# Optimization experiments

Hardware: AMD Instinct MI355X
Metric: run time of the kernel (lower is better)

## Reference

```python
import jax, jax.numpy as jnp
import numpy as np

D_MODEL = 1024
N_HEADS = 16
HEAD_DIM = D_MODEL // N_HEADS
SCALE = HEAD_DIM ** -0.5
MASK_FILL = -10000.0


def setup_inputs() -> dict:
    key = jax.random.key(0)
    ks = jax.random.split(key, 12)
    B, L, D = 2, 2048, D_MODEL
    inv = 1.0 / np.sqrt(D)
    inp = {
        "query": jax.random.normal(ks[0], (B, L, D), jnp.float32),
        "key": jax.random.normal(ks[1], (B, L, D), jnp.float32),
        "value": jax.random.normal(ks[2], (B, L, D), jnp.float32),
        "Wq": jax.random.normal(ks[3], (D, D), jnp.float32) * inv,
        "bq": jnp.zeros((D,), jnp.float32),
        "Wk": jax.random.normal(ks[4], (D, D), jnp.float32) * inv,
        "bk": jnp.zeros((D,), jnp.float32),
        "Wv": jax.random.normal(ks[5], (D, D), jnp.float32) * inv,
        "bv": jnp.zeros((D,), jnp.float32),
        "Wo": jax.random.normal(ks[6], (D, D), jnp.float32) * inv,
        "bo": jnp.zeros((D,), jnp.float32),
        "valid_mask": jax.random.randint(ks[7], (B, L), 0, 2).astype(jnp.bool_),
    }
    return inp


def reference(query, key, value, Wq, bq, Wk, bk, Wv, bv, Wo, bo, valid_mask):
    B, Lq, D = query.shape
    Lk = key.shape[1]
    H, HD = N_HEADS, HEAD_DIM
    # torch.nn.Linear: y = x @ W.T + b
    Q = (query @ Wq.T + bq).reshape(B, Lq, H, HD).transpose(0, 2, 1, 3)  # [B,H,Lq,HD]
    K = (key @ Wk.T + bk).reshape(B, Lk, H, HD).transpose(0, 2, 1, 3)    # [B,H,Lk,HD]
    V = (value @ Wv.T + bv).reshape(B, Lk, H, HD).transpose(0, 2, 1, 3)  # [B,H,Lk,HD]
    scores = jnp.einsum("bhqd,bhkd->bhqk", Q, K) * SCALE
    scores = jnp.where(valid_mask[:, None, None, :], scores, MASK_FILL)
    weights = jax.nn.softmax(scores, axis=-1)  # dropout is identity at inference
    out = jnp.einsum("bhqk,bhkd->bhqd", weights, V)
    out = out.transpose(0, 2, 1, 3).reshape(B, Lq, D)
    out = out @ Wo.T + bo
    # zero rows of fully-invalid batches
    gate = jnp.any(valid_mask, axis=1).astype(out.dtype)[:, None, None]
    return out * gate
```

## Files before the change

### kernel.cpp

```cpp
#include <hip/hip_runtime.h>
#include <hip/hip_bf16.h>

typedef __hip_bfloat16 bf16;
typedef __attribute__((ext_vector_type(8))) short s8v;
typedef __attribute__((ext_vector_type(4))) float f4v;

#define LOG2E 1.44269504088896340736f
#define CSCALE (0.125f * LOG2E)
#define MASK_B2 (-14426.950408889634f)
#define NEG_BIG (-30000.0f)

#define BB 2
#define LL 2048
#define DD 1024
#define HH 16
#define HD 64
#define MTOT 4096
#define PER_T 4194304

struct alignas(8) B4 { bf16 v[4]; };

__device__ __forceinline__ void async_cp16(const bf16* g, bf16* l) {
    __builtin_amdgcn_global_load_lds(
        (const __attribute__((address_space(1))) void*)g,
        (__attribute__((address_space(3))) void*)l, 16, 0, 0);
}

struct CvtArgs {
    const float* src[7];
    bf16* dst[7];
    int n[7];
};

__global__ __launch_bounds__(256) void cvt_kernel(CvtArgs args) {
    const int which = blockIdx.y;
    const float* __restrict__ src = args.src[which];
    bf16* __restrict__ dst = args.dst[which];
    const int n4 = args.n[which] >> 2;
    const int stride = gridDim.x * 256;
    for (int i = blockIdx.x * 256 + threadIdx.x; i < n4; i += stride) {
        const float4 f = ((const float4*)src)[i];
        B4 o;
        o.v[0] = __float2bfloat16(f.x);
        o.v[1] = __float2bfloat16(f.y);
        o.v[2] = __float2bfloat16(f.z);
        o.v[3] = __float2bfloat16(f.w);
        ((B4*)dst)[i] = o;
    }
}

struct QkvArgs {
    const bf16* A[3];
    const bf16* W[3];
    const float* bias[3];
    bf16* out[3];
};

template <int FUSED>
__global__ __launch_bounds__(256) void gemm128(QkvArgs qa,
                                               const bf16* __restrict__ Ao,
                                               const bf16* __restrict__ Wo_,
                                               const float* __restrict__ bo_,
                                               float* __restrict__ out_f,
                                               const int* __restrict__ mask) {
    __shared__ bf16 sA[128 * 64];
    __shared__ bf16 sB[128 * 64];
    __shared__ int sgate;

    const int which = FUSED ? blockIdx.z : 0;
    const bf16* __restrict__ A = FUSED ? qa.A[which] : Ao;
    const bf16* __restrict__ W = FUSED ? qa.W[which] : Wo_;
    const float* __restrict__ bias = FUSED ? qa.bias[which] : bo_;
    bf16* __restrict__ out_bf = FUSED ? qa.out[which] : nullptr;

    const int lane = threadIdx.x & 63;
    const int w = threadIdx.x >> 6;
    const int lr = lane & 15;
    const int quad = lane >> 4;
    const int wr = w >> 1, wc = w & 1;
    const int rbase = blockIdx.x * 128;
    const int cbase = blockIdx.y * 128;
    const int dma_r = lane >> 3;
    const int dma_cc = ((lane & 7) ^ dma_r) * 8;

    if (!FUSED) {
        if (threadIdx.x == 0) sgate = 0;
        __syncthreads();
        const int b_ = rbase >> 11;
        int any = 0;
        for (int i = threadIdx.x; i < LL; i += 256) any |= mask[b_ * LL + i];
        if (any) sgate = 1;
    }

    f4v acc[4][4] = {};
    for (int kt = 0; kt < DD / 64; kt++) {
        const int k0 = kt * 64;
        __syncthreads();
#pragma unroll
        for (int t = 0; t < 4; t++) {
            const int g = w * 4 + t;
            async_cp16(A + (size_t)(rbase + g * 8 + dma_r) * DD + k0 + dma_cc,
                       &sA[g * 512]);
            async_cp16(W + (size_t)(cbase + g * 8 + dma_r) * DD + k0 + dma_cc,
                       &sB[g * 512]);
        }
        __syncthreads();
#pragma unroll
        for (int s = 0; s < 2; s++) {
            s8v a[4], b[4];
#pragma unroll
            for (int i = 0; i < 4; i++) {
                const int row = wr * 64 + i * 16 + lr;
                a[i] = *(const s8v*)&sA[row * 64 + (((s * 4 + quad) ^ (row & 7)) * 8)];
            }
#pragma unroll
            for (int j = 0; j < 4; j++) {
                const int row = wc * 64 + j * 16 + lr;
                b[j] = *(const s8v*)&sB[row * 64 + (((s * 4 + quad) ^ (row & 7)) * 8)];
            }
#pragma unroll
            for (int i = 0; i < 4; i++)
#pragma unroll
                for (int j = 0; j < 4; j++)
                    acc[i][j] = __builtin_amdgcn_mfma_f32_16x16x32_bf16(a[i], b[j], acc[i][j], 0, 0, 0);
        }
    }

    const float gatef = (!FUSED) ? (sgate ? 1.0f : 0.0f) : 1.0f;

#pragma unroll
    for (int j = 0; j < 4; j++) {
        const int n = cbase + wc * 64 + j * 16 + lr;
        const float bv = bias[n];
#pragma unroll
        for (int i = 0; i < 4; i++) {
#pragma unroll
            for (int r = 0; r < 4; r++) {
                const int m = rbase + wr * 64 + i * 16 + quad * 4 + r;
                const float v = acc[i][j][r] + bv;
                if (!FUSED) {
                    out_f[(size_t)m * DD + n] = v * gatef;
                } else {
                    const int b_ = m >> 11, l = m & (LL - 1);
                    const int h = n >> 6, hd = n & 63;
                    if (which == 2)
                        out_bf[(((size_t)(b_ * HH + h)) * HD + hd) * LL + l] = __float2bfloat16(v);
                    else
                        out_bf[(((size_t)(b_ * HH + h)) * LL + l) * HD + hd] = __float2bfloat16(v);
                }
            }
        }
    }
}

__global__ __launch_bounds__(512) void attn_kernel(const bf16* __restrict__ Q,
                                                   const bf16* __restrict__ K,
                                                   const bf16* __restrict__ Vt,
                                                   const int* __restrict__ mask,
                                                   bf16* __restrict__ Aout) {
    __shared__ bf16 sK[2][64 * 64];
    __shared__ bf16 sV[2][64 * 64];
    __shared__ bf16 sP[8][16 * 72];
    __shared__ float sBias[LL];

    const int lane = threadIdx.x & 63;
    const int w = threadIdx.x >> 6;
    const int lr = lane & 15;
    const int quad = lane >> 4;

    const int bid = blockIdx.x;
    const int qb = bid & 15;
    const int h = (bid >> 4) & 15;
    const int b = bid >> 8;

    const size_t head_off = ((size_t)(b * HH + h)) * LL * HD;
    const bf16* Qh = Q + head_off;
    const bf16* Kh = K + head_off;
    const bf16* Vh = Vt + head_off;
    const int q0 = qb * 128 + w * 16;

    const int dma_r = lane >> 3;
    const int dma_cc = ((lane & 7) ^ dma_r) * 8;
    const int sw = lr & 7;

    {
        const int* mb = mask + b * LL;
        for (int i = threadIdx.x; i < LL; i += 512)
            sBias[i] = mb[i] ? 0.0f : MASK_B2;
        async_cp16(Kh + (size_t)(w * 8 + dma_r) * HD + dma_cc, &sK[0][w * 512]);
        async_cp16(Vh + (size_t)(w * 8 + dma_r) * LL + dma_cc, &sV[0][w * 512]);
    }
    __syncthreads();

    const s8v aq0 = *(const s8v*)(Qh + (size_t)(q0 + lr) * HD + quad * 8);
    const s8v aq1 = *(const s8v*)(Qh + (size_t)(q0 + lr) * HD + 32 + quad * 8);

    bf16* sPw = &sP[w][0];
    f4v O[4] = {};
    float mrun = NEG_BIG, lrun = 0.0f;

    int asrc[4];
#pragma unroll
    for (int r = 0; r < 4; r++) asrc[r] = (lane & 48) | (quad * 4 + r);

    for (int kt = 0; kt < LL / 64; kt++) {
        const int kbase = kt * 64;
        const bf16* kb = &sK[kt & 1][0];
        const bf16* vb = &sV[kt & 1][0];

        if (kt < LL / 64 - 1) {
            const int nb = (kt + 1) & 1;
            async_cp16(Kh + (size_t)(kbase + 64 + w * 8 + dma_r) * HD + dma_cc,
                       &sK[nb][w * 512]);
            async_cp16(Vh + (size_t)(w * 8 + dma_r) * LL + kbase + 64 + dma_cc,
                       &sV[nb][w * 512]);
        }

        f4v T[4];
#pragma unroll
        for (int j = 0; j < 4; j++) {
            const int row = 16 * j + lr;
            const s8v kb0 = *(const s8v*)&kb[row * 64 + ((quad ^ sw) * 8)];
            const s8v kb1 = *(const s8v*)&kb[row * 64 + (((quad + 4) ^ sw) * 8)];
            f4v t = {};
            t = __builtin_amdgcn_mfma_f32_16x16x32_bf16(kb0, aq0, t, 0, 0, 0);
            T[j] = __builtin_amdgcn_mfma_f32_16x16x32_bf16(kb1, aq1, t, 0, 0, 0);
        }

        s8v v0[4], v1[4];
#pragma unroll
        for (int dt = 0; dt < 4; dt++) {
            const int vrow = dt * 16 + lr;
            v0[dt] = *(const s8v*)&vb[vrow * 64 + ((quad ^ sw) * 8)];
            v1[dt] = *(const s8v*)&vb[vrow * 64 + (((quad + 4) ^ sw) * 8)];
        }

        float mloc = NEG_BIG;
#pragma unroll
        for (int j = 0; j < 4; j++) {
            const f4v bj = *(const f4v*)&sBias[kbase + j * 16 + quad * 4];
#pragma unroll
            for (int r = 0; r < 4; r++) {
                T[j][r] = T[j][r] * CSCALE + bj[r];
                mloc = fmaxf(mloc, T[j][r]);
            }
        }
        mloc = fmaxf(mloc, __shfl_xor(mloc, 16));
        mloc = fmaxf(mloc, __shfl_xor(mloc, 32));

        if (__any(mloc > mrun)) {
            const float mnew = fmaxf(mrun, mloc);
            const float alphaq = exp2f(mrun - mnew);
            mrun = mnew;
            lrun *= alphaq;
            float aB[4];
#pragma unroll
            for (int r = 0; r < 4; r++) aB[r] = __shfl(alphaq, asrc[r]);
#pragma unroll
            for (int dt = 0; dt < 4; dt++)
#pragma unroll
                for (int r = 0; r < 4; r++) O[dt][r] *= aB[r];
        }

        float ls = 0.0f;
#pragma unroll
        for (int j = 0; j < 4; j++)
#pragma unroll
            for (int r = 0; r < 4; r++) {
                const float e = exp2f(T[j][r] - mrun);
                T[j][r] = e;
                ls += e;
            }
        ls += __shfl_xor(ls, 16);
        ls += __shfl_xor(ls, 32);
        lrun += ls;

        asm volatile("" ::: "memory");
#pragma unroll
        for (int j = 0; j < 4; j++) {
            B4 pk;
            pk.v[0] = __float2bfloat16(T[j][0]);
            pk.v[1] = __float2bfloat16(T[j][1]);
            pk.v[2] = __float2bfloat16(T[j][2]);
            pk.v[3] = __float2bfloat16(T[j][3]);
            *(B4*)&sPw[lr * 72 + j * 16 + quad * 4] = pk;
        }
        asm volatile("s_waitcnt lgkmcnt(0)" ::: "memory");
        const s8v pa0 = *(const s8v*)(sPw + lr * 72 + quad * 8);
        const s8v pa1 = *(const s8v*)(sPw + lr * 72 + 32 + quad * 8);

#pragma unroll
        for (int dt = 0; dt < 4; dt++) {
            O[dt] = __builtin_amdgcn_mfma_f32_16x16x32_bf16(pa0, v0[dt], O[dt], 0, 0, 0);
            O[dt] = __builtin_amdgcn_mfma_f32_16x16x32_bf16(pa1, v1[dt], O[dt], 0, 0, 0);
        }

        __syncthreads();
    }

    const float linv = 1.0f / lrun;
    float lB[4];
#pragma unroll
    for (int r = 0; r < 4; r++) lB[r] = __shfl(linv, asrc[r]);
#pragma unroll
    for (int dt = 0; dt < 4; dt++)
#pragma unroll
        for (int r = 0; r < 4; r++) {
            const int q = q0 + quad * 4 + r;
            Aout[((size_t)(b * LL + q)) * DD + h * HD + dt * 16 + lr] =
                __float2bfloat16(O[dt][r] * lB[r]);
        }
}

extern "C" void kernel_launch(void* const* d_in, const int* in_sizes, int n_in,
                              void* d_out, int out_size, void* d_ws, size_t ws_size,
                              hipStream_t stream) {
    const float* query = (const float*)d_in[0];
    const float* key   = (const float*)d_in[1];
    const float* value = (const float*)d_in[2];
    const float* Wq = (const float*)d_in[3];
    const float* bq = (const float*)d_in[4];
    const float* Wk = (const float*)d_in[5];
    const float* bk = (const float*)d_in[6];
    const float* Wv = (const float*)d_in[7];
    const float* bv = (const float*)d_in[8];
    const float* Wo = (const float*)d_in[9];
    const float* bo = (const float*)d_in[10];
    const int* mask = (const int*)d_in[11];

    bf16* base = (bf16*)d_ws;
    bf16* qx = base;
    bf16* kx = qx + PER_T;
    bf16* vx = kx + PER_T;
    bf16* wq = vx + PER_T;
    bf16* wk = wq + DD * DD;
    bf16* wv = wk + DD * DD;
    bf16* wo = wv + DD * DD;
    bf16* Qs = wo + DD * DD;
    bf16* Ks = Qs + PER_T;
    bf16* Vst = Ks + PER_T;
    bf16* aws = Vst + PER_T;

    CvtArgs ca;
    ca.src[0] = query; ca.dst[0] = qx; ca.n[0] = PER_T;
    ca.src[1] = key;   ca.dst[1] = kx; ca.n[1] = PER_T;
    ca.src[2] = value; ca.dst[2] = vx; ca.n[2] = PER_T;
    ca.src[3] = Wq;    ca.dst[3] = wq; ca.n[3] = DD * DD;
    ca.src[4] = Wk;    ca.dst[4] = wk; ca.n[4] = DD * DD;
    ca.src[5] = Wv;    ca.dst[5] = wv; ca.n[5] = DD * DD;
    ca.src[6] = Wo;    ca.dst[6] = wo; ca.n[6] = DD * DD;
    cvt_kernel<<<dim3(1024, 7), 256, 0, stream>>>(ca);

    QkvArgs qa;
    qa.A[0] = qx; qa.W[0] = wq; qa.bias[0] = bq; qa.out[0] = Qs;
    qa.A[1] = kx; qa.W[1] = wk; qa.bias[1] = bk; qa.out[1] = Ks;
    qa.A[2] = vx; qa.W[2] = wv; qa.bias[2] = bv; qa.out[2] = Vst;

    gemm128<1><<<dim3(MTOT / 128, DD / 128, 3), 256, 0, stream>>>(
        qa, nullptr, nullptr, nullptr, nullptr, nullptr);

    attn_kernel<<<BB * HH * (LL / 128), 512, 0, stream>>>(Qs, Ks, Vst, mask, aws);

    QkvArgs dummy{};
    gemm128<0><<<dim3(MTOT / 128, DD / 128, 1), 256, 0, stream>>>(
        dummy, aws, wo, bo, (float*)d_out, mask);
}
```

Before: 267.3 us.

## Vectorize GEMM epilogue stores via MFMA operand swap and LDS-staged transpose

Swaps the MFMA operands so each lane holds four consecutive output columns, which lets the Wo projection write float4 stores and the Q/K projections stage tiles through padded LDS. The V projection, whose output is transposed, is also staged through LDS. All head-layout outputs are then written back as 16-byte coalesced rows instead of scattered 2-byte stores. This costs an extra LDS round trip and a barrier in the epilogue and reuses the operand LDS buffer.

Result: faster. 258.1 us (-3.4%).

```diff
diff --git a/kernel.cpp b/kernel.cpp
--- a/kernel.cpp
+++ b/kernel.cpp
@@ -56,22 +56,16 @@
     bf16* out[3];
 };
 
-template <int FUSED>
-__global__ __launch_bounds__(256) void gemm128(QkvArgs qa,
-                                               const bf16* __restrict__ Ao,
-                                               const bf16* __restrict__ Wo_,
-                                               const float* __restrict__ bo_,
-                                               float* __restrict__ out_f,
-                                               const int* __restrict__ mask) {
-    __shared__ bf16 sA[128 * 64];
-    __shared__ bf16 sB[128 * 64];
-    __shared__ int sgate;
-
-    const int which = FUSED ? blockIdx.z : 0;
-    const bf16* __restrict__ A = FUSED ? qa.A[which] : Ao;
-    const bf16* __restrict__ W = FUSED ? qa.W[which] : Wo_;
-    const float* __restrict__ bias = FUSED ? qa.bias[which] : bo_;
-    bf16* __restrict__ out_bf = FUSED ? qa.out[which] : nullptr;
+template <int FUSED, int SWAP>
+__device__ __forceinline__ void gemm_body(const bf16* __restrict__ A,
+                                          const bf16* __restrict__ W,
+                                          const float* __restrict__ bias,
+                                          bf16* __restrict__ out_bf,
+                                          float* __restrict__ out_f,
+                                          float gatef, char* smem) {
+    bf16* sA = (bf16*)smem;
+    bf16* sB = (bf16*)(smem + 128 * 64 * 2);
+    bf16* sE = (bf16*)smem;
 
     const int lane = threadIdx.x & 63;
     const int w = threadIdx.x >> 6;
@@ -83,15 +77,6 @@
     const int dma_r = lane >> 3;
     const int dma_cc = ((lane & 7) ^ dma_r) * 8;
 
-    if (!FUSED) {
-        if (threadIdx.x == 0) sgate = 0;
-        __syncthreads();
-        const int b_ = rbase >> 11;
-        int any = 0;
-        for (int i = threadIdx.x; i < LL; i += 256) any |= mask[b_ * LL + i];
-        if (any) sgate = 1;
-    }
-
     f4v acc[4][4] = {};
     for (int kt = 0; kt < DD / 64; kt++) {
         const int k0 = kt * 64;
@@ -122,34 +107,126 @@
             for (int i = 0; i < 4; i++)
 #pragma unroll
                 for (int j = 0; j < 4; j++)
-                    acc[i][j] = __builtin_amdgcn_mfma_f32_16x16x32_bf16(a[i], b[j], acc[i][j], 0, 0, 0);
-        }
-    }
-
-    const float gatef = (!FUSED) ? (sgate ? 1.0f : 0.0f) : 1.0f;
-
-#pragma unroll
-    for (int j = 0; j < 4; j++) {
-        const int n = cbase + wc * 64 + j * 16 + lr;
-        const float bv = bias[n];
-#pragma unroll
-        for (int i = 0; i < 4; i++) {
-#pragma unroll
-            for (int r = 0; r < 4; r++) {
-                const int m = rbase + wr * 64 + i * 16 + quad * 4 + r;
-                const float v = acc[i][j][r] + bv;
-                if (!FUSED) {
-                    out_f[(size_t)m * DD + n] = v * gatef;
-                } else {
-                    const int b_ = m >> 11, l = m & (LL - 1);
-                    const int h = n >> 6, hd = n & 63;
-                    if (which == 2)
-                        out_bf[(((size_t)(b_ * HH + h)) * HD + hd) * LL + l] = __float2bfloat16(v);
-                    else
-                        out_bf[(((size_t)(b_ * HH + h)) * LL + l) * HD + hd] = __float2bfloat16(v);
-                }
-            }
-        }
+                    acc[i][j] = SWAP
+                        ? __builtin_amdgcn_mfma_f32_16x16x32_bf16(b[j], a[i], acc[i][j], 0, 0, 0)
+                        : __builtin_amdgcn_mfma_f32_16x16x32_bf16(a[i], b[j], acc[i][j], 0, 0, 0);
+        }
+    }
+    __syncthreads();
+
+    if (FUSED == 0) {
+#pragma unroll
+        for (int j = 0; j < 4; j++) {
+            const int n = cbase + wc * 64 + j * 16 + quad * 4;
+            const f4v bv = *(const f4v*)&bias[n];
+#pragma unroll
+            for (int i = 0; i < 4; i++) {
+                const int m = rbase + wr * 64 + i * 16 + lr;
+                float4 o;
+                o.x = (acc[i][j][0] + bv[0]) * gatef;
+                o.y = (acc[i][j][1] + bv[1]) * gatef;
+                o.z = (acc[i][j][2] + bv[2]) * gatef;
+                o.w = (acc[i][j][3] + bv[3]) * gatef;
+                *(float4*)&out_f[(size_t)m * DD + n] = o;
+            }
+        }
+        return;
+    }
+
+    if (SWAP) {
+#pragma unroll
+        for (int j = 0; j < 4; j++) {
+            const int n_loc = wc * 64 + j * 16 + quad * 4;
+            const f4v bv = *(const f4v*)&bias[cbase + n_loc];
+#pragma unroll
+            for (int i = 0; i < 4; i++) {
+                const int m_loc = wr * 64 + i * 16 + lr;
+                B4 pk;
+                pk.v[0] = __float2bfloat16(acc[i][j][0] + bv[0]);
+                pk.v[1] = __float2bfloat16(acc[i][j][1] + bv[1]);
+                pk.v[2] = __float2bfloat16(acc[i][j][2] + bv[2]);
+                pk.v[3] = __float2bfloat16(acc[i][j][3] + bv[3]);
+                *(B4*)&sE[m_loc * 136 + n_loc] = pk;
+            }
+        }
+        __syncthreads();
+        const int tid = threadIdx.x;
+        const int mr_ = tid >> 4;
+        const int n0 = (tid & 15) * 8;
+#pragma unroll
+        for (int ro = 0; ro < 8; ro++) {
+            const int m_loc = ro * 16 + mr_;
+            const s8v vv = *(const s8v*)&sE[m_loc * 136 + n0];
+            const int m = rbase + m_loc;
+            const int n = cbase + n0;
+            const int b_ = m >> 11, l = m & (LL - 1);
+            const int h = n >> 6, hd = n & 63;
+            *(s8v*)&out_bf[(((size_t)(b_ * HH + h)) * LL + l) * HD + hd] = vv;
+        }
+    } else {
+#pragma unroll
+        for (int j = 0; j < 4; j++) {
+            const int n_loc = wc * 64 + j * 16 + lr;
+            const float bv = bias[cbase + n_loc];
+#pragma unroll
+            for (int i = 0; i < 4; i++) {
+                const int m0 = wr * 64 + i * 16 + quad * 4;
+                B4 pk;
+                pk.v[0] = __float2bfloat16(acc[i][j][0] + bv);
+                pk.v[1] = __float2bfloat16(acc[i][j][1] + bv);
+                pk.v[2] = __float2bfloat16(acc[i][j][2] + bv);
+                pk.v[3] = __float2bfloat16(acc[i][j][3] + bv);
+                *(B4*)&sE[n_loc * 136 + m0] = pk;
+            }
+        }
+        __syncthreads();
+        const int tid = threadIdx.x;
+#pragma unroll
+        for (int ro = 0; ro < 8; ro++) {
+            const int n_loc = ro * 16 + (tid >> 4);
+            const int m0 = (tid & 15) * 8;
+            const s8v vv = *(const s8v*)&sE[n_loc * 136 + m0];
+            const int n = cbase + n_loc;
+            const int m = rbase + m0;
+            const int b_ = m >> 11, l = m & (LL - 1);
+            const int h = n >> 6, hd = n & 63;
+            *(s8v*)&out_bf[(((size_t)(b_ * HH + h)) * HD + hd) * LL + l] = vv;
+        }
+    }
+}
+
+template <int FUSED>
+__global__ __launch_bounds__(256) void gemm128(QkvArgs qa,
+                                               const bf16* __restrict__ Ao,
+                                               const bf16* __restrict__ Wo_,
+                                               const float* __restrict__ bo_,
+                                               float* __restrict__ out_f,
+                                               const int* __restrict__ mask) {
+    __shared__ __align__(16) char smem[128 * 136 * 2];
+    __shared__ int sgate;
+
+    float gatef = 1.0f;
+    if (!FUSED) {
+        if (threadIdx.x == 0) sgate = 0;
+        __syncthreads();
+        const int b_ = (int)(blockIdx.x * 128) >> 11;
+        int any = 0;
+        for (int i = threadIdx.x; i < LL; i += 256) any |= mask[b_ * LL + i];
+        if (any) sgate = 1;
+        __syncthreads();
+        gatef = sgate ? 1.0f : 0.0f;
+    }
+
+    if (FUSED) {
+        const int which = blockIdx.z;
+        if (which != 2)
+            gemm_body<1, 1>(qa.A[which], qa.W[which], qa.bias[which],
+                            qa.out[which], nullptr, 1.0f, smem);
+        else
+            gemm_body<1, 0>(qa.A[2], qa.W[2], qa.bias[2],
+                            qa.out[2], nullptr, 1.0f, smem);
+    } else {
+        gemm_body<0, 1>(Ao, Wo_, bo_, nullptr, out_f, gatef, smem);
     }
 }
 
```
